# Optimization experiments

Hardware: AMD Instinct MI355X
Metric: run time of the kernel (lower is better)

The kernel has to match this reference:

```python
import jax, jax.numpy as jnp
import numpy as np

FIR = (1.0, 3.0, 3.0, 1.0)

def _fir_kernel():
    k = jnp.array(FIR, dtype=jnp.float32)
    k = jnp.outer(k, k)
    return k / jnp.sum(k)  # gain = 1

def setup_inputs() -> dict:
    key = jax.random.key(0)
    k1, k2, k3 = jax.random.split(key, 3)
    N, C, H, W = 8, 512, 64, 64
    return {
        "hidden_states": jax.random.normal(k1, (N, C, H, W), jnp.float32),
        "weight": jax.random.normal(k2, (512, 512, 3, 3), jnp.float32) * 0.02,
        "bias": jax.random.normal(k3, (512,), jnp.float32) * 0.01,
    }

def reference(hidden_states, weight, bias):
    # FirDownsample2D forward, use_conv=True, factor=2, fir_kernel=(1,3,3,1).
    # pad_value = kH - factor + (convW - 1) = 4 - 2 + 2 = 4 -> pad = (2, 2)
    k = _fir_kernel()  # [4,4], normalized
    C = hidden_states.shape[1]
    # upfirdn2d_native with up=1, down=1: pad spatially then per-channel
    # cross-correlation with the FLIPPED kernel (== true convolution).
    kf = jnp.flip(k, (0, 1)).astype(hidden_states.dtype)
    kf = jnp.broadcast_to(kf[None, None], (C, 1, 4, 4))  # depthwise [C,1,4,4]
    y = jax.lax.conv_general_dilated(
        hidden_states, kf, window_strides=(1, 1), padding=[(2, 2), (2, 2)],
        dimension_numbers=("NCHW", "OIHW", "NCHW"), feature_group_count=C)
    # y: [N, C, H+1, W+1]; fused 3x3 conv, stride=factor=2, no padding.
    out = jax.lax.conv_general_dilated(
        y, weight, window_strides=(2, 2), padding="VALID",
        dimension_numbers=("NCHW", "OIHW", "NCHW"))  # [N, Cout, H//2, W//2]
    return out + bias[None, :, None, None]
```

## Files before the change

### kernel.cpp

```cpp
#include <hip/hip_runtime.h>
#include <stdint.h>

#define CI 512
#define CO 512
#define HI 64
#define WI 64
#define HY 65
#define NB 8

typedef __bf16 bf16x8 __attribute__((ext_vector_type(8)));
typedef float f32x4 __attribute__((ext_vector_type(4)));

__device__ __forceinline__ unsigned short f2bf(float f) {
  unsigned int u = __float_as_uint(f);
  return (unsigned short)((u + 0x7fffu + ((u >> 16) & 1u)) >> 16);
}

__device__ __forceinline__ void async16(void* lds, const void* g) {
  __builtin_amdgcn_global_load_lds(
      (const __attribute__((address_space(1))) uint32_t*)g,
      (__attribute__((address_space(3))) uint32_t*)lds, 16, 0, 0);
}

#define CT 32
#define RT 13

__global__ __launch_bounds__(256) void fir_kernel(const float* __restrict__ x,
                                                  unsigned short* __restrict__ yt) {
  __shared__ float raw[CT][WI + 1];
  __shared__ float hrow[4][HY][CT];

  const int tid = threadIdx.x;
  const int bid = blockIdx.x;
  const int n = bid / 80;
  const int rem = bid % 80;
  const int c0 = (rem / 5) * CT;
  const int r0 = (rem % 5) * RT;

  const float* xb = x + ((size_t)n * CI + c0) * (HI * WI);

  const int lc = tid >> 3;
  const int lq = tid & 7;
  const int c = tid & (CT - 1);
  const int sb = tid >> 5;

  auto stage = [&](int hr) {
    __syncthreads();
    if ((unsigned)hr < (unsigned)HI) {
      const float* rowp = xb + ((size_t)lc * HI + hr) * WI;
      float4 a = *(const float4*)&rowp[lq * 4];
      float4 b = *(const float4*)&rowp[(lq + 8) * 4];
      raw[lc][lq * 4 + 0] = a.x; raw[lc][lq * 4 + 1] = a.y;
      raw[lc][lq * 4 + 2] = a.z; raw[lc][lq * 4 + 3] = a.w;
      raw[lc][(lq + 8) * 4 + 0] = b.x; raw[lc][(lq + 8) * 4 + 1] = b.y;
      raw[lc][(lq + 8) * 4 + 2] = b.z; raw[lc][(lq + 8) * 4 + 3] = b.w;
    }
    __syncthreads();
    const int slot = hr & 3;
    if ((unsigned)hr < (unsigned)HI) {
#pragma unroll
      for (int k = 0; k < 9; k++) {
        const int s = sb + (k << 3);
        if (s < HY) {
          float v = 0.f;
          if (s >= 2) v += raw[c][s - 2];
          if (s >= 1) v += 3.f * raw[c][s - 1];
          if (s <= 63) v += 3.f * raw[c][s];
          if (s <= 62) v += raw[c][s + 1];
          hrow[slot][s][c] = v;
        }
      }
    } else {
#pragma unroll
      for (int k = 0; k < 9; k++) {
        const int s = sb + (k << 3);
        if (s < HY) hrow[slot][s][c] = 0.f;
      }
    }
  };

  stage(r0 - 2);
  stage(r0 - 1);
  stage(r0);

  for (int i = 0; i < RT; i++) {
    const int r = r0 + i;
    stage(r + 1);
    __syncthreads();
    const int q0 = (r - 2) & 3, q1 = (r - 1) & 3, q2 = r & 3, q3 = (r + 1) & 3;
    unsigned short* yo = yt + (((size_t)n * HY + r) * HY) * CI + c0 + c;
#pragma unroll
    for (int k = 0; k < 9; k++) {
      const int s = sb + (k << 3);
      if (s < HY) {
        const float y = (hrow[q0][s][c] + 3.f * hrow[q1][s][c] +
                         3.f * hrow[q2][s][c] + hrow[q3][s][c]) * (1.f / 64.f);
        yo[(size_t)s * CI] = f2bf(y);
      }
    }
  }
}

__global__ __launch_bounds__(256) void wt_kernel(const float* __restrict__ w,
                                                 unsigned short* __restrict__ wtb) {
  const int gid = blockIdx.x * 256 + threadIdx.x;
  const int ci = gid & (CI - 1);
  const int co = gid >> 9;
  const float* src = w + ((size_t)co * CI + ci) * 9;
#pragma unroll
  for (int t = 0; t < 9; t++) {
    wtb[((size_t)t * CO + co) * CI + ci] = f2bf(src[t]);
  }
}

__global__ __launch_bounds__(256) void init_kernel(const float* __restrict__ bias,
                                                   float* __restrict__ out) {
  const int gid = blockIdx.x * 256 + threadIdx.x;
  const float bv = bias[(gid >> 8) & 511];
  float4 v = {bv, bv, bv, bv};
  *(float4*)(out + (size_t)gid * 4) = v;
}

__global__ __launch_bounds__(256, 3) void conv_kernel(
    const unsigned short* __restrict__ wtb,
    const unsigned short* __restrict__ yt,
    float* __restrict__ out) {
  __shared__ unsigned short Alds[2][64 * 64];
  __shared__ unsigned short Blds[2][128 * 64];

  const int tid = threadIdx.x;
  const int xcd = blockIdx.x & 7;
  const int j = blockIdx.x >> 3;
  const int pos_tile = xcd * 8 + (j >> 4);
  const int variant = j & 15;
  const int co_t = (variant >> 1) << 6;
  const int split = variant & 1;
  const int ks0 = split * 36;
  const int m0 = pos_tile << 7;
  const int n = m0 >> 10;
  const int w = tid >> 6, l = tid & 63;

  size_t aoff[2];
#pragma unroll
  for (int i = 0; i < 2; i++) {
    const int cch = i * 256 + w * 64 + l;
    const int row = cch >> 3, s = cch & 7;
    aoff[i] = (size_t)(co_t + row) * CI + ((s ^ (row & 7)) << 3);
  }
  size_t boff[4];
#pragma unroll
  for (int i = 0; i < 4; i++) {
    const int cch = i * 256 + w * 64 + l;
    const int p = cch >> 3, s = cch & 7;
    const int pos = m0 + p;
    const int ho = (pos & 1023) >> 5, wo = pos & 31;
    boff[i] = (((size_t)n * HY + 2 * ho) * HY + 2 * wo) * CI + ((s ^ (p & 7)) << 3);
  }

  auto stage = [&](int b, int ks) {
    const int tap = ks >> 3;
    const int ci0 = (ks & 7) << 6;
    const int kh = tap / 3, kw = tap - kh * 3;
    const size_t ka = (size_t)tap * (CO * CI) + ci0;
    const size_t kb = (size_t)(kh * HY + kw) * CI + ci0;
    unsigned short* Ab = &Alds[b][0];
    unsigned short* Bb = &Blds[b][0];
#pragma unroll
    for (int i = 0; i < 2; i++)
      async16(Ab + (size_t)(i * 256 + w * 64 + l) * 8, wtb + ka + aoff[i]);
#pragma unroll
    for (int i = 0; i < 4; i++)
      async16(Bb + (size_t)(i * 256 + w * 64 + l) * 8, yt + kb + boff[i]);
  };

  const int wco = (w >> 1) << 5;
  const int wpos = (w & 1) << 6;
  const int ll = l & 15, kg = l >> 4;
  const int a7 = ll & 7;

  int aidx[2][2], bidx[4][2];
#pragma unroll
  for (int m = 0; m < 2; m++)
#pragma unroll
    for (int kk = 0; kk < 2; kk++)
      aidx[m][kk] = (wco + m * 16 + ll) * 64 + ((((kk << 2) | kg) ^ a7) << 3);
#pragma unroll
  for (int nf = 0; nf < 4; nf++)
#pragma unroll
    for (int kk = 0; kk < 2; kk++)
      bidx[nf][kk] = (wpos + nf * 16 + ll) * 64 + ((((kk << 2) | kg) ^ a7) << 3);

  f32x4 acc[2][4] = {};

  stage(0, ks0);
  __syncthreads();

  int cur = 0;
  for (int t = 0; t < 36; t++) {
    if (t < 35) stage(cur ^ 1, ks0 + t + 1);
    const unsigned short* Ac = &Alds[cur][0];
    const unsigned short* Bc = &Blds[cur][0];
#pragma unroll
    for (int kk = 0; kk < 2; kk++) {
      const bf16x8 a0 = *(const bf16x8*)(Ac + aidx[0][kk]);
      const bf16x8 a1 = *(const bf16x8*)(Ac + aidx[1][kk]);
      const bf16x8 b0 = *(const bf16x8*)(Bc + bidx[0][kk]);
      const bf16x8 b1 = *(const bf16x8*)(Bc + bidx[1][kk]);
      const bf16x8 b2 = *(const bf16x8*)(Bc + bidx[2][kk]);
      const bf16x8 b3 = *(const bf16x8*)(Bc + bidx[3][kk]);
      acc[0][0] = __builtin_amdgcn_mfma_f32_16x16x32_bf16(a0, b0, acc[0][0], 0, 0, 0);
      acc[0][1] = __builtin_amdgcn_mfma_f32_16x16x32_bf16(a0, b1, acc[0][1], 0, 0, 0);
      acc[0][2] = __builtin_amdgcn_mfma_f32_16x16x32_bf16(a0, b2, acc[0][2], 0, 0, 0);
      acc[0][3] = __builtin_amdgcn_mfma_f32_16x16x32_bf16(a0, b3, acc[0][3], 0, 0, 0);
      acc[1][0] = __builtin_amdgcn_mfma_f32_16x16x32_bf16(a1, b0, acc[1][0], 0, 0, 0);
      acc[1][1] = __builtin_amdgcn_mfma_f32_16x16x32_bf16(a1, b1, acc[1][1], 0, 0, 0);
      acc[1][2] = __builtin_amdgcn_mfma_f32_16x16x32_bf16(a1, b2, acc[1][2], 0, 0, 0);
      acc[1][3] = __builtin_amdgcn_mfma_f32_16x16x32_bf16(a1, b3, acc[1][3], 0, 0, 0);
    }
    __syncthreads();
    cur ^= 1;
  }

#pragma unroll
  for (int i = 0; i < 2; i++) {
#pragma unroll
    for (int r = 0; r < 4; r++) {
      const int co = co_t + wco + i * 16 + kg * 4 + r;
      float* orow = out + ((size_t)n * CO + co) * 1024;
#pragma unroll
      for (int jf = 0; jf < 4; jf++) {
        const int pos = m0 + wpos + jf * 16 + ll;
        atomicAdd(orow + (pos & 1023), acc[i][jf][r]);
      }
    }
  }
}

extern "C" void kernel_launch(void* const* d_in, const int* in_sizes, int n_in,
                              void* d_out, int out_size, void* d_ws, size_t ws_size,
                              hipStream_t stream) {
  const float* x = (const float*)d_in[0];
  const float* w = (const float*)d_in[1];
  const float* bias = (const float*)d_in[2];
  float* out = (float*)d_out;

  unsigned short* yt = (unsigned short*)d_ws;
  unsigned short* wtb = yt + (size_t)NB * HY * HY * CI;

  fir_kernel<<<NB * (CI / CT) * 5, 256, 0, stream>>>(x, yt);
  wt_kernel<<<(CO * CI) / 256, 256, 0, stream>>>(w, wtb);
  init_kernel<<<4096, 256, 0, stream>>>(bias, out);
  conv_kernel<<<1024, 256, 0, stream>>>(wtb, yt, out);
}
```

Before: 119.5 us.

## Enlarge conv tile to 128x128 and prefetch FIR input rows into registers

The conv kernel tile grows from 64 to 128 output channels per block, so each wave computes a 64x64 sub-tile with 16 MFMA accumulators and the grid halves to 512 blocks. This raises reuse of the staged activation tile and cuts redundant B loads, at the cost of more registers and LDS and a drop in occupancy hint from 3 to 2 blocks. Offsets move to 32-bit integers. Separately, the FIR kernel now loads the next input row into registers before the barrier, overlapping global latency with the horizontal filter work.

```diff
diff --git a/kernel.cpp b/kernel.cpp
--- a/kernel.cpp
+++ b/kernel.cpp
@@ -44,17 +44,24 @@
   const int c = tid & (CT - 1);
   const int sb = tid >> 5;
 
-  auto stage = [&](int hr) {
-    __syncthreads();
+  float4 pA, pB;
+  auto preload = [&](int hr) {
     if ((unsigned)hr < (unsigned)HI) {
       const float* rowp = xb + ((size_t)lc * HI + hr) * WI;
-      float4 a = *(const float4*)&rowp[lq * 4];
-      float4 b = *(const float4*)&rowp[(lq + 8) * 4];
-      raw[lc][lq * 4 + 0] = a.x; raw[lc][lq * 4 + 1] = a.y;
-      raw[lc][lq * 4 + 2] = a.z; raw[lc][lq * 4 + 3] = a.w;
-      raw[lc][(lq + 8) * 4 + 0] = b.x; raw[lc][(lq + 8) * 4 + 1] = b.y;
-      raw[lc][(lq + 8) * 4 + 2] = b.z; raw[lc][(lq + 8) * 4 + 3] = b.w;
-    }
+      pA = *(const float4*)&rowp[lq * 4];
+      pB = *(const float4*)&rowp[(lq + 8) * 4];
+    }
+  };
+
+  auto stage = [&](int hr) {
+    __syncthreads();
+    if ((unsigned)hr < (unsigned)HI) {
+      raw[lc][lq * 4 + 0] = pA.x; raw[lc][lq * 4 + 1] = pA.y;
+      raw[lc][lq * 4 + 2] = pA.z; raw[lc][lq * 4 + 3] = pA.w;
+      raw[lc][(lq + 8) * 4 + 0] = pB.x; raw[lc][(lq + 8) * 4 + 1] = pB.y;
+      raw[lc][(lq + 8) * 4 + 2] = pB.z; raw[lc][(lq + 8) * 4 + 3] = pB.w;
+    }
+    preload(hr + 1);
     __syncthreads();
     const int slot = hr & 3;
     if ((unsigned)hr < (unsigned)HI) {
@@ -79,6 +86,7 @@
     }
   };
 
+  preload(r0 - 2);
   stage(r0 - 2);
   stage(r0 - 1);
   stage(r0);
@@ -121,66 +129,60 @@
   *(float4*)(out + (size_t)gid * 4) = v;
 }
 
-__global__ __launch_bounds__(256, 3) void conv_kernel(
+__global__ __launch_bounds__(256, 2) void conv_kernel(
     const unsigned short* __restrict__ wtb,
     const unsigned short* __restrict__ yt,
     float* __restrict__ out) {
-  __shared__ unsigned short Alds[2][64 * 64];
+  __shared__ unsigned short Alds[2][128 * 64];
   __shared__ unsigned short Blds[2][128 * 64];
 
   const int tid = threadIdx.x;
   const int xcd = blockIdx.x & 7;
   const int j = blockIdx.x >> 3;
-  const int pos_tile = xcd * 8 + (j >> 4);
-  const int variant = j & 15;
-  const int co_t = (variant >> 1) << 6;
+  const int pos_tile = xcd * 8 + (j >> 3);
+  const int variant = j & 7;
+  const int co_t = (variant >> 1) << 7;
   const int split = variant & 1;
   const int ks0 = split * 36;
   const int m0 = pos_tile << 7;
   const int n = m0 >> 10;
   const int w = tid >> 6, l = tid & 63;
 
-  size_t aoff[2];
-#pragma unroll
-  for (int i = 0; i < 2; i++) {
-    const int cch = i * 256 + w * 64 + l;
-    const int row = cch >> 3, s = cch & 7;
-    aoff[i] = (size_t)(co_t + row) * CI + ((s ^ (row & 7)) << 3);
-  }
-  size_t boff[4];
+  uint32_t aoff[4], boff[4];
 #pragma unroll
   for (int i = 0; i < 4; i++) {
-    const int cch = i * 256 + w * 64 + l;
-    const int p = cch >> 3, s = cch & 7;
-    const int pos = m0 + p;
+    const int ch = tid + i * 256;
+    const int row = ch >> 3, s = ch & 7;
+    aoff[i] = (uint32_t)((co_t + row) * CI + ((s ^ (row & 7)) << 3));
+    const int pos = m0 + row;
     const int ho = (pos & 1023) >> 5, wo = pos & 31;
-    boff[i] = (((size_t)n * HY + 2 * ho) * HY + 2 * wo) * CI + ((s ^ (p & 7)) << 3);
+    boff[i] = (uint32_t)(((n * HY + 2 * ho) * HY + 2 * wo) * CI + ((s ^ (row & 7)) << 3));
   }
 
   auto stage = [&](int b, int ks) {
     const int tap = ks >> 3;
     const int ci0 = (ks & 7) << 6;
     const int kh = tap / 3, kw = tap - kh * 3;
-    const size_t ka = (size_t)tap * (CO * CI) + ci0;
-    const size_t kb = (size_t)(kh * HY + kw) * CI + ci0;
+    const unsigned short* ws = wtb + (size_t)tap * (CO * CI) + ci0;
+    const unsigned short* ys = yt + (size_t)(kh * HY + kw) * CI + ci0;
     unsigned short* Ab = &Alds[b][0];
     unsigned short* Bb = &Blds[b][0];
 #pragma unroll
-    for (int i = 0; i < 2; i++)
-      async16(Ab + (size_t)(i * 256 + w * 64 + l) * 8, wtb + ka + aoff[i]);
-#pragma unroll
     for (int i = 0; i < 4; i++)
-      async16(Bb + (size_t)(i * 256 + w * 64 + l) * 8, yt + kb + boff[i]);
+      async16(Ab + (size_t)(tid + i * 256) * 8, ws + aoff[i]);
+#pragma unroll
+    for (int i = 0; i < 4; i++)
+      async16(Bb + (size_t)(tid + i * 256) * 8, ys + boff[i]);
   };
 
-  const int wco = (w >> 1) << 5;
+  const int wco = (w >> 1) << 6;
   const int wpos = (w & 1) << 6;
   const int ll = l & 15, kg = l >> 4;
   const int a7 = ll & 7;
 
-  int aidx[2][2], bidx[4][2];
-#pragma unroll
-  for (int m = 0; m < 2; m++)
+  int aidx[4][2], bidx[4][2];
+#pragma unroll
+  for (int m = 0; m < 4; m++)
 #pragma unroll
     for (int kk = 0; kk < 2; kk++)
       aidx[m][kk] = (wco + m * 16 + ll) * 64 + ((((kk << 2) | kg) ^ a7) << 3);
@@ -190,7 +192,7 @@
     for (int kk = 0; kk < 2; kk++)
       bidx[nf][kk] = (wpos + nf * 16 + ll) * 64 + ((((kk << 2) | kg) ^ a7) << 3);
 
-  f32x4 acc[2][4] = {};
+  f32x4 acc[4][4] = {};
 
   stage(0, ks0);
   __syncthreads();
@@ -204,33 +206,35 @@
     for (int kk = 0; kk < 2; kk++) {
       const bf16x8 a0 = *(const bf16x8*)(Ac + aidx[0][kk]);
       const bf16x8 a1 = *(const bf16x8*)(Ac + aidx[1][kk]);
+      const bf16x8 a2 = *(const bf16x8*)(Ac + aidx[2][kk]);
+      const bf16x8 a3 = *(const bf16x8*)(Ac + aidx[3][kk]);
       const bf16x8 b0 = *(const bf16x8*)(Bc + bidx[0][kk]);
       const bf16x8 b1 = *(const bf16x8*)(Bc + bidx[1][kk]);
       const bf16x8 b2 = *(const bf16x8*)(Bc + bidx[2][kk]);
       const bf16x8 b3 = *(const bf16x8*)(Bc + bidx[3][kk]);
-      acc[0][0] = __builtin_amdgcn_mfma_f32_16x16x32_bf16(a0, b0, acc[0][0], 0, 0, 0);
-      acc[0][1] = __builtin_amdgcn_mfma_f32_16x16x32_bf16(a0, b1, acc[0][1], 0, 0, 0);
-      acc[0][2] = __builtin_amdgcn_mfma_f32_16x16x32_bf16(a0, b2, acc[0][2], 0, 0, 0);
-      acc[0][3] = __builtin_amdgcn_mfma_f32_16x16x32_bf16(a0, b3, acc[0][3], 0, 0, 0);
-      acc[1][0] = __builtin_amdgcn_mfma_f32_16x16x32_bf16(a1, b0, acc[1][0], 0, 0, 0);
-      acc[1][1] = __builtin_amdgcn_mfma_f32_16x16x32_bf16(a1, b1, acc[1][1], 0, 0, 0);
-      acc[1][2] = __builtin_amdgcn_mfma_f32_16x16x32_bf16(a1, b2, acc[1][2], 0, 0, 0);
-      acc[1][3] = __builtin_amdgcn_mfma_f32_16x16x32_bf16(a1, b3, acc[1][3], 0, 0, 0);
+#pragma unroll
+      for (int m = 0; m < 4; m++) {
+        const bf16x8 am = (m == 0) ? a0 : (m == 1) ? a1 : (m == 2) ? a2 : a3;
+        acc[m][0] = __builtin_amdgcn_mfma_f32_16x16x32_bf16(am, b0, acc[m][0], 0, 0, 0);
+        acc[m][1] = __builtin_amdgcn_mfma_f32_16x16x32_bf16(am, b1, acc[m][1], 0, 0, 0);
+        acc[m][2] = __builtin_amdgcn_mfma_f32_16x16x32_bf16(am, b2, acc[m][2], 0, 0, 0);
+        acc[m][3] = __builtin_amdgcn_mfma_f32_16x16x32_bf16(am, b3, acc[m][3], 0, 0, 0);
+      }
     }
     __syncthreads();
     cur ^= 1;
   }
 
 #pragma unroll
-  for (int i = 0; i < 2; i++) {
+  for (int m = 0; m < 4; m++) {
 #pragma unroll
     for (int r = 0; r < 4; r++) {
-      const int co = co_t + wco + i * 16 + kg * 4 + r;
+      const int co = co_t + wco + m * 16 + kg * 4 + r;
       float* orow = out + ((size_t)n * CO + co) * 1024;
 #pragma unroll
-      for (int jf = 0; jf < 4; jf++) {
-        const int pos = m0 + wpos + jf * 16 + ll;
-        atomicAdd(orow + (pos & 1023), acc[i][jf][r]);
+      for (int nf = 0; nf < 4; nf++) {
+        const int pos = m0 + wpos + nf * 16 + ll;
+        atomicAdd(orow + (pos & 1023), acc[m][nf][r]);
       }
     }
   }
@@ -250,5 +254,5 @@
   fir_kernel<<<NB * (CI / CT) * 5, 256, 0, stream>>>(x, yt);
   wt_kernel<<<(CO * CI) / 256, 256, 0, stream>>>(w, wtb);
   init_kernel<<<4096, 256, 0, stream>>>(bias, out);
-  conv_kernel<<<1024, 256, 0, stream>>>(wtb, yt, out);
-}
+  conv_kernel<<<512, 256, 0, stream>>>(wtb, yt, out);
+}
```

New measurement: 106.1 us. -11.2%, faster.
